# Optimization experiments

Measured on AMD Instinct MI355X. Metric: run time of the kernel, lower is better.

The kernel has to match this reference:

```python
import jax, jax.numpy as jnp
import numpy as np
import math

B, S, IN_DIM, ORIG_DIM, EMBED, HEADS = 8, 1024, 512, 64, 512, 8
HEAD_DIM = EMBED // HEADS


def setup_inputs() -> dict:
    key = jax.random.key(0)
    ks = jax.random.split(key, 4)
    # xavier-uniform-ish init for weights, zero bias (matches _reset_parameters)
    def xavier(k, shape):
        fan_in, fan_out = shape[1], shape[0]
        lim = math.sqrt(6.0 / (fan_in + fan_out))
        return jax.random.uniform(k, shape, jnp.float32, -lim, lim)
    return {
        "x": jax.random.normal(ks[0], (B, S, IN_DIM), jnp.float32),
        "inp": jax.random.normal(ks[1], (B, S, ORIG_DIM), jnp.float32),
        "W_qkv": xavier(ks[2], (3 * EMBED, IN_DIM + ORIG_DIM)),
        "b_qkv": jnp.zeros((3 * EMBED,), jnp.float32),
        "W_o": xavier(ks[3], (EMBED, EMBED)),
        "b_o": jnp.zeros((EMBED,), jnp.float32),
    }


def reference(x, inp, W_qkv, b_qkv, W_o, b_o):
    b, s, _ = x.shape
    xc = jnp.concatenate([x, inp], axis=2)              # [B,S,IN+ORIG]
    qkv = xc @ W_qkv.T + b_qkv                          # [B,S,3E]
    qkv = qkv.reshape(b, s, HEADS, 3 * HEAD_DIM).transpose(0, 2, 1, 3)  # [B,H,S,3d]
    q, k, v = jnp.split(qkv, 3, axis=-1)                # each [B,H,S,d]
    logits = jnp.einsum("bhqd,bhkd->bhqk", q, k) / math.sqrt(HEAD_DIM)
    attention = jax.nn.softmax(logits, axis=-1)         # [B,H,S,S]
    values = jnp.einsum("bhqk,bhkd->bhqd", attention, v)
    values = values.transpose(0, 2, 1, 3).reshape(b, s, EMBED)
    o = values @ W_o.T + b_o                            # [B,S,E]
    return o, attention
```

## Files before the change

### kernel.cpp

```cpp
#include <hip/hip_runtime.h>

typedef __bf16 bf16x8 __attribute__((ext_vector_type(8)));
typedef __bf16 bf16x4 __attribute__((ext_vector_type(4)));
typedef float f32x4 __attribute__((ext_vector_type(4)));

#define MFMA16(a,b,c) __builtin_amdgcn_mfma_f32_16x16x32_bf16((a),(b),(c),0,0,0)

__device__ __forceinline__ void gload_lds16(const void* g, void* l) {
    __builtin_amdgcn_global_load_lds(
        (const __attribute__((address_space(1))) void*)g,
        (__attribute__((address_space(3))) void*)l, 16, 0, 0);
}


__global__ __launch_bounds__(256) void k_convert(
    const float* __restrict__ x, const float* __restrict__ inp,
    const float* __restrict__ Wqkv, const float* __restrict__ Wo,
    __bf16* __restrict__ xc, __bf16* __restrict__ wq, __bf16* __restrict__ wo)
{
    const unsigned C1 = 589824u;
    const unsigned C2 = 110592u;
    unsigned i = blockIdx.x * 256u + threadIdx.x;
    if (i < C1) {
        unsigned e = i * 8u;
        unsigned m = e / 576u, k = e - m * 576u;
        const float* p = (k < 512u) ? x + (size_t)m * 512u + k
                                    : inp + (size_t)m * 64u + (k - 512u);
        f32x4 a = *(const f32x4*)p, b = *(const f32x4*)(p + 4);
        bf16x8 o;
#pragma unroll
        for (int j = 0; j < 4; ++j) { o[j] = (__bf16)a[j]; o[j + 4] = (__bf16)b[j]; }
        *(bf16x8*)&xc[e] = o;
    } else if (i < C1 + C2) {
        unsigned e = (i - C1) * 8u;
        f32x4 a = *(const f32x4*)&Wqkv[e], b = *(const f32x4*)&Wqkv[e + 4];
        bf16x8 o;
#pragma unroll
        for (int j = 0; j < 4; ++j) { o[j] = (__bf16)a[j]; o[j + 4] = (__bf16)b[j]; }
        *(bf16x8*)&wq[e] = o;
    } else {
        unsigned e = (i - C1 - C2) * 8u;
        f32x4 a = *(const f32x4*)&Wo[e], b = *(const f32x4*)&Wo[e + 4];
        bf16x8 o;
#pragma unroll
        for (int j = 0; j < 4; ++j) { o[j] = (__bf16)a[j]; o[j + 4] = (__bf16)b[j]; }
        *(bf16x8*)&wo[e] = o;
    }
}

__global__ __launch_bounds__(256) void k_qkv_gemm(
    const __bf16* __restrict__ A, const __bf16* __restrict__ W,
    const float* __restrict__ bias,
    __bf16* __restrict__ q_ws, __bf16* __restrict__ k_ws, __bf16* __restrict__ vt_ws)
{
    const int K = 576;
    __shared__ __align__(16) __bf16 As[128][32];
    __shared__ __align__(16) __bf16 Bs[128][32];
    int m0 = blockIdx.x * 128, n0 = blockIdx.y * 128;
    int t = threadIdx.x, w = t >> 6, l = t & 63;
    int lo = l & 15, hi = l >> 4;
    int wr = w >> 1, wc = w & 1;

    const __bf16* gA = A + (size_t)(m0 + w * 16 + (l >> 2)) * K + (l & 3) * 8;
    const __bf16* gB = W + (size_t)(n0 + w * 16 + (l >> 2)) * K + (l & 3) * 8;
    char* lA = (char*)&As[0][0] + w * 1024;
    char* lB = (char*)&Bs[0][0] + w * 1024;

    f32x4 acc[4][4] = {};
    for (int k0 = 0; k0 < K; k0 += 32) {
        gload_lds16(gA + k0, lA);
        gload_lds16(gA + 64 * K + k0, lA + 4096);
        gload_lds16(gB + k0, lB);
        gload_lds16(gB + 64 * K + k0, lB + 4096);
        __syncthreads();
        bf16x8 af[4], bq[4];
#pragma unroll
        for (int mi = 0; mi < 4; ++mi) af[mi] = *(const bf16x8*)&As[wr * 64 + mi * 16 + lo][hi * 8];
#pragma unroll
        for (int ni = 0; ni < 4; ++ni) bq[ni] = *(const bf16x8*)&Bs[wc * 64 + ni * 16 + lo][hi * 8];
#pragma unroll
        for (int mi = 0; mi < 4; ++mi)
#pragma unroll
            for (int ni = 0; ni < 4; ++ni)
                acc[mi][ni] = MFMA16(af[mi], bq[ni], acc[mi][ni]);
        __syncthreads();
    }

#pragma unroll
    for (int ni = 0; ni < 4; ++ni) {
        int n = n0 + wc * 64 + ni * 16 + lo;
        int h = n / 192, jj = n % 192, part = jj >> 6, d = jj & 63;
        float bn = bias[n];
#pragma unroll
        for (int mi = 0; mi < 4; ++mi)
#pragma unroll
            for (int j = 0; j < 4; ++j) {
                int m = m0 + wr * 64 + mi * 16 + hi * 4 + j;
                float v = acc[mi][ni][j] + bn;
                int b = m >> 10, s = m & 1023;
                size_t bh = (size_t)(b * 8 + h);
                if (part == 0)      q_ws[(bh * 1024 + s) * 64 + d] = (__bf16)(v * 0.125f);
                else if (part == 1) k_ws[(bh * 1024 + s) * 64 + d] = (__bf16)v;
                else                vt_ws[(bh * 64 + d) * 1024 + s] = (__bf16)v;
            }
    }
}

__global__ __launch_bounds__(256, 4) void k_attn(
    const __bf16* __restrict__ q_ws, const __bf16* __restrict__ k_ws,
    const __bf16* __restrict__ vt_ws,
    float* __restrict__ att_out, __bf16* __restrict__ values)
{
    __shared__ __align__(16) __bf16 Klds[2][64][76];
    __shared__ __align__(16) __bf16 Pl[2][4][16][76];

    int bid = blockIdx.x;
    int nid = (bid & 7) * 128 + (bid >> 3);
    int bh = nid >> 4, qt = nid & 15;
    int t = threadIdx.x, w = t >> 6, l = t & 63;
    int lo = l & 15, hi = l >> 4;
    int q0 = qt * 64 + w * 16;

    const __bf16* Qg = q_ws + ((size_t)bh * 1024 + q0 + lo) * 64 + hi * 8;
    bf16x8 qa0 = *(const bf16x8*)Qg;
    bf16x8 qa1 = *(const bf16x8*)(Qg + 32);

    const __bf16* Kb = k_ws + (size_t)bh * 65536;
    int srow = t >> 2, scol = (t & 3) * 16;
    const __bf16* gK = Kb + (size_t)srow * 64 + scol;
    bf16x8 r0, r1;

#define STAGE_LOAD(c)  { const __bf16* p_ = gK + (size_t)(c) * 4096; \
                         r0 = *(const bf16x8*)p_; r1 = *(const bf16x8*)(p_ + 8); }
#define STAGE_WRITE(b) { *(bf16x8*)&Klds[b][srow][scol] = r0; \
                         *(bf16x8*)&Klds[b][srow][scol + 8] = r1; }
#define SCHUNK(b, s)   _Pragma("unroll") \
                       for (int kk = 0; kk < 4; ++kk) { \
                           bf16x8 kb0 = *(const bf16x8*)&Klds[b][kk * 16 + lo][hi * 8]; \
                           bf16x8 kb1 = *(const bf16x8*)&Klds[b][kk * 16 + lo][hi * 8 + 32]; \
                           f32x4 a_ = {}; \
                           a_ = MFMA16(qa0, kb0, a_); \
                           a_ = MFMA16(qa1, kb1, a_); \
                           s[kk] = a_; \
                       }

    f32x4 lmx = { -3.4e38f, -3.4e38f, -3.4e38f, -3.4e38f };
    f32x4 lsum = {};
    STAGE_LOAD(0); STAGE_WRITE(0);
    __syncthreads();
    for (int c = 0; c < 16; ++c) {
        if (c < 15) STAGE_LOAD(c + 1);
        f32x4 s[4];
        SCHUNK(c & 1, s);
#pragma unroll
        for (int j = 0; j < 4; ++j) {
            float cm = fmaxf(fmaxf(s[0][j], s[1][j]), fmaxf(s[2][j], s[3][j]));
            float nm = fmaxf(lmx[j], cm);
            float a = __expf(s[0][j] - nm) + __expf(s[1][j] - nm)
                    + __expf(s[2][j] - nm) + __expf(s[3][j] - nm);
            lsum[j] = lsum[j] * __expf(lmx[j] - nm) + a;
            lmx[j] = nm;
        }
        if (c < 15) STAGE_WRITE((c + 1) & 1);
        __syncthreads();
    }
    f32x4 gmx = lmx;
#pragma unroll
    for (int off = 1; off < 16; off <<= 1)
#pragma unroll
        for (int j = 0; j < 4; ++j) gmx[j] = fmaxf(gmx[j], __shfl_xor(gmx[j], off));
    f32x4 part;
#pragma unroll
    for (int j = 0; j < 4; ++j) part[j] = lsum[j] * __expf(lmx[j] - gmx[j]);
#pragma unroll
    for (int off = 1; off < 16; off <<= 1)
#pragma unroll
        for (int j = 0; j < 4; ++j) part[j] += __shfl_xor(part[j], off);
    f32x4 ginv;
#pragma unroll
    for (int j = 0; j < 4; ++j) ginv[j] = 1.f / part[j];

    float* gattW = att_out + ((size_t)bh * 1024 + q0) * 1024;
    const __bf16* Vb = vt_ws + (size_t)bh * 65536 + (size_t)(w * 16 + lo) * 1024 + hi * 8;
    f32x4 oacc[4] = {};

    STAGE_LOAD(0); STAGE_WRITE(0);
    __syncthreads();
    for (int c = 0; c < 16; ++c) {
        if (c < 15) STAGE_LOAD(c + 1);
        f32x4 s[4];
        SCHUNK(c & 1, s);
#pragma unroll
        for (int kk = 0; kk < 4; ++kk)
#pragma unroll
            for (int j = 0; j < 4; ++j) {
                float p = __expf(s[kk][j] - gmx[j]) * ginv[j];
                gattW[(size_t)(hi * 4 + j) * 1024 + c * 64 + kk * 16 + lo] = p;
                Pl[c & 1][w][hi * 4 + j][kk * 16 + lo] = (__bf16)p;
            }
        if (c > 0) {
            int pb = (c - 1) & 1;
            const __bf16* vp = Vb + (size_t)(c - 1) * 64;
            bf16x8 vb0 = *(const bf16x8*)vp;
            bf16x8 vb1 = *(const bf16x8*)(vp + 32);
#pragma unroll
            for (int g = 0; g < 4; ++g) {
                bf16x8 pa0 = *(const bf16x8*)&Pl[pb][g][lo][hi * 8];
                bf16x8 pa1 = *(const bf16x8*)&Pl[pb][g][lo][hi * 8 + 32];
                oacc[g] = MFMA16(pa0, vb0, oacc[g]);
                oacc[g] = MFMA16(pa1, vb1, oacc[g]);
            }
        }
        if (c < 15) STAGE_WRITE((c + 1) & 1);
        __syncthreads();
    }
    {
        const __bf16* vp = Vb + (size_t)15 * 64;
        bf16x8 vb0 = *(const bf16x8*)vp;
        bf16x8 vb1 = *(const bf16x8*)(vp + 32);
#pragma unroll
        for (int g = 0; g < 4; ++g) {
            bf16x8 pa0 = *(const bf16x8*)&Pl[1][g][lo][hi * 8];
            bf16x8 pa1 = *(const bf16x8*)&Pl[1][g][lo][hi * 8 + 32];
            oacc[g] = MFMA16(pa0, vb0, oacc[g]);
            oacc[g] = MFMA16(pa1, vb1, oacc[g]);
        }
    }

    int b = bh >> 3, h = bh & 7;
#pragma unroll
    for (int g = 0; g < 4; ++g)
#pragma unroll
        for (int j = 0; j < 4; ++j)
            values[((size_t)b * 1024 + qt * 64 + g * 16 + hi * 4 + j) * 512
                   + h * 64 + w * 16 + lo] = (__bf16)oacc[g][j];
#undef STAGE_LOAD
#undef STAGE_WRITE
#undef SCHUNK
}

__global__ __launch_bounds__(256) void k_out_gemm(
    const __bf16* __restrict__ A, const __bf16* __restrict__ W,
    const float* __restrict__ bias, float* __restrict__ out)
{
    const int K = 512;
    __shared__ __align__(16) __bf16 As[128][32];
    __shared__ __align__(16) __bf16 Bs[128][32];
    int m0 = blockIdx.x * 128, n0 = blockIdx.y * 128;
    int t = threadIdx.x, w = t >> 6, l = t & 63;
    int lo = l & 15, hi = l >> 4;
    int wr = w >> 1, wc = w & 1;

    const __bf16* gA = A + (size_t)(m0 + w * 16 + (l >> 2)) * K + (l & 3) * 8;
    const __bf16* gB = W + (size_t)(n0 + w * 16 + (l >> 2)) * K + (l & 3) * 8;
    char* lA = (char*)&As[0][0] + w * 1024;
    char* lB = (char*)&Bs[0][0] + w * 1024;

    f32x4 acc[4][4] = {};
    for (int k0 = 0; k0 < K; k0 += 32) {
        gload_lds16(gA + k0, lA);
        gload_lds16(gA + 64 * K + k0, lA + 4096);
        gload_lds16(gB + k0, lB);
        gload_lds16(gB + 64 * K + k0, lB + 4096);
        __syncthreads();
        bf16x8 af[4], bq[4];
#pragma unroll
        for (int mi = 0; mi < 4; ++mi) af[mi] = *(const bf16x8*)&As[wr * 64 + mi * 16 + lo][hi * 8];
#pragma unroll
        for (int ni = 0; ni < 4; ++ni) bq[ni] = *(const bf16x8*)&Bs[wc * 64 + ni * 16 + lo][hi * 8];
#pragma unroll
        for (int mi = 0; mi < 4; ++mi)
#pragma unroll
            for (int ni = 0; ni < 4; ++ni)
                acc[mi][ni] = MFMA16(af[mi], bq[ni], acc[mi][ni]);
        __syncthreads();
    }

#pragma unroll
    for (int ni = 0; ni < 4; ++ni) {
        int n = n0 + wc * 64 + ni * 16 + lo;
        float bn = bias[n];
#pragma unroll
        for (int mi = 0; mi < 4; ++mi)
#pragma unroll
            for (int j = 0; j < 4; ++j) {
                int m = m0 + wr * 64 + mi * 16 + hi * 4 + j;
                out[(size_t)m * 512 + n] = acc[mi][ni][j] + bn;
            }
    }
}

extern "C" void kernel_launch(void* const* d_in, const int* in_sizes, int n_in,
                              void* d_out, int out_size, void* d_ws, size_t ws_size,
                              hipStream_t stream)
{
    const float* x    = (const float*)d_in[0];
    const float* inp  = (const float*)d_in[1];
    const float* Wqkv = (const float*)d_in[2];
    const float* bqkv = (const float*)d_in[3];
    const float* Wo   = (const float*)d_in[4];
    const float* bo   = (const float*)d_in[5];

    float* out_o   = (float*)d_out;
    float* out_att = out_o + (size_t)8 * 1024 * 512;

    char* ws = (char*)d_ws;
    __bf16* xc    = (__bf16*)(ws + 0);
    __bf16* wq    = (__bf16*)(ws + 9437184);
    __bf16* wo    = (__bf16*)(ws + 11206656);
    __bf16* q_ws  = (__bf16*)(ws + 11730944);
    __bf16* k_ws  = (__bf16*)(ws + 20119552);
    __bf16* vt_ws = (__bf16*)(ws + 28508160);
    __bf16* vals  = (__bf16*)(ws + 36896768);

    k_convert<<<2864, 256, 0, stream>>>(x, inp, Wqkv, Wo, xc, wq, wo);
    k_qkv_gemm<<<dim3(64, 12), 256, 0, stream>>>(xc, wq, bqkv, q_ws, k_ws, vt_ws);
    k_attn<<<1024, 256, 0, stream>>>(q_ws, k_ws, vt_ws, out_att, vals);
    k_out_gemm<<<dim3(64, 4), 256, 0, stream>>>(vals, wo, bo, out_o);
}
```

Measured before the change: 132.3 us.

## Process two query tiles per attention block, fusing tile B's stats pass with tile A's emit pass

Each attention block now handles two 64-row query tiles of the same head and makes three K sweeps instead of four. Tile B's online max/sum pass is merged into tile A's probability-emit and PV pass, so one K staging serves both. The grid is halved to 512 blocks and the occupancy hint drops from 4 to 2 blocks per CU to allow more registers. The risk is lower parallelism: fewer blocks and fewer waves to hide the latency of the large fp32 attention-matrix stores.

```diff
diff --git a/kernel.cpp b/kernel.cpp
--- a/kernel.cpp
+++ b/kernel.cpp
@@ -106,7 +106,7 @@
     }
 }
 
-__global__ __launch_bounds__(256, 4) void k_attn(
+__global__ __launch_bounds__(256, 2) void k_attn(
     const __bf16* __restrict__ q_ws, const __bf16* __restrict__ k_ws,
     const __bf16* __restrict__ vt_ws,
     float* __restrict__ att_out, __bf16* __restrict__ values)
@@ -115,15 +115,19 @@
     __shared__ __align__(16) __bf16 Pl[2][4][16][76];
 
     int bid = blockIdx.x;
-    int nid = (bid & 7) * 128 + (bid >> 3);
-    int bh = nid >> 4, qt = nid & 15;
+    int nid = (bid & 7) * 64 + (bid >> 3);
+    int bh = nid >> 3, pr = nid & 7;
     int t = threadIdx.x, w = t >> 6, l = t & 63;
     int lo = l & 15, hi = l >> 4;
-    int q0 = qt * 64 + w * 16;
-
-    const __bf16* Qg = q_ws + ((size_t)bh * 1024 + q0 + lo) * 64 + hi * 8;
-    bf16x8 qa0 = *(const bf16x8*)Qg;
-    bf16x8 qa1 = *(const bf16x8*)(Qg + 32);
+    int q0A = pr * 128 + w * 16;
+    int q0B = q0A + 64;
+
+    const __bf16* QgA = q_ws + ((size_t)bh * 1024 + q0A + lo) * 64 + hi * 8;
+    const __bf16* QgB = q_ws + ((size_t)bh * 1024 + q0B + lo) * 64 + hi * 8;
+    bf16x8 qaA0 = *(const bf16x8*)QgA;
+    bf16x8 qaA1 = *(const bf16x8*)(QgA + 32);
+    bf16x8 qaB0 = *(const bf16x8*)QgB;
+    bf16x8 qaB1 = *(const bf16x8*)(QgB + 32);
 
     const __bf16* Kb = k_ws + (size_t)bh * 65536;
     int srow = t >> 2, scol = (t & 3) * 16;
@@ -134,7 +138,7 @@
                          r0 = *(const bf16x8*)p_; r1 = *(const bf16x8*)(p_ + 8); }
 #define STAGE_WRITE(b) { *(bf16x8*)&Klds[b][srow][scol] = r0; \
                          *(bf16x8*)&Klds[b][srow][scol + 8] = r1; }
-#define SCHUNK(b, s)   _Pragma("unroll") \
+#define SCHUNK(b, s, qa0, qa1) _Pragma("unroll") \
                        for (int kk = 0; kk < 4; ++kk) { \
                            bf16x8 kb0 = *(const bf16x8*)&Klds[b][kk * 16 + lo][hi * 8]; \
                            bf16x8 kb1 = *(const bf16x8*)&Klds[b][kk * 16 + lo][hi * 8 + 32]; \
@@ -143,100 +147,126 @@
                            a_ = MFMA16(qa1, kb1, a_); \
                            s[kk] = a_; \
                        }
+#define ONLINE(s, lmx, lsum) _Pragma("unroll") \
+                       for (int j = 0; j < 4; ++j) { \
+                           float cm = fmaxf(fmaxf(s[0][j], s[1][j]), fmaxf(s[2][j], s[3][j])); \
+                           float nm = fmaxf(lmx[j], cm); \
+                           float a = __expf(s[0][j] - nm) + __expf(s[1][j] - nm) \
+                                   + __expf(s[2][j] - nm) + __expf(s[3][j] - nm); \
+                           lsum[j] = lsum[j] * __expf(lmx[j] - nm) + a; \
+                           lmx[j] = nm; \
+                       }
+#define REDUCE(lmx, lsum, gmx, ginv) { \
+                       gmx = lmx; \
+                       _Pragma("unroll") \
+                       for (int off = 1; off < 16; off <<= 1) \
+                           _Pragma("unroll") \
+                           for (int j = 0; j < 4; ++j) gmx[j] = fmaxf(gmx[j], __shfl_xor(gmx[j], off)); \
+                       f32x4 part_; \
+                       _Pragma("unroll") \
+                       for (int j = 0; j < 4; ++j) part_[j] = lsum[j] * __expf(lmx[j] - gmx[j]); \
+                       _Pragma("unroll") \
+                       for (int off = 1; off < 16; off <<= 1) \
+                           _Pragma("unroll") \
+                           for (int j = 0; j < 4; ++j) part_[j] += __shfl_xor(part_[j], off); \
+                       _Pragma("unroll") \
+                       for (int j = 0; j < 4; ++j) ginv[j] = 1.f / part_[j]; }
+#define EMIT(s, gmx, ginv, gatt, pb) _Pragma("unroll") \
+                       for (int kk = 0; kk < 4; ++kk) \
+                           _Pragma("unroll") \
+                           for (int j = 0; j < 4; ++j) { \
+                               float p = __expf(s[kk][j] - gmx[j]) * ginv[j]; \
+                               gatt[(size_t)(hi * 4 + j) * 1024 + c * 64 + kk * 16 + lo] = p; \
+                               Pl[pb][w][hi * 4 + j][kk * 16 + lo] = (__bf16)p; \
+                           }
+#define PV(cc, oacc)   { int pb_ = (cc) & 1; \
+                         const __bf16* vp_ = Vb + (size_t)(cc) * 64; \
+                         bf16x8 vb0 = *(const bf16x8*)vp_; \
+                         bf16x8 vb1 = *(const bf16x8*)(vp_ + 32); \
+                         _Pragma("unroll") \
+                         for (int g = 0; g < 4; ++g) { \
+                             bf16x8 pa0 = *(const bf16x8*)&Pl[pb_][g][lo][hi * 8]; \
+                             bf16x8 pa1 = *(const bf16x8*)&Pl[pb_][g][lo][hi * 8 + 32]; \
+                             oacc[g] = MFMA16(pa0, vb0, oacc[g]); \
+                             oacc[g] = MFMA16(pa1, vb1, oacc[g]); \
+                         } }
+#define VSTORE(qt, oacc) _Pragma("unroll") \
+                       for (int g = 0; g < 4; ++g) \
+                           _Pragma("unroll") \
+                           for (int j = 0; j < 4; ++j) \
+                               values[((size_t)(bh >> 3) * 1024 + (qt) * 64 + g * 16 + hi * 4 + j) * 512 \
+                                      + (bh & 7) * 64 + w * 16 + lo] = (__bf16)oacc[g][j];
+
+    const __bf16* Vb = vt_ws + (size_t)bh * 65536 + (size_t)(w * 16 + lo) * 1024 + hi * 8;
+    float* gattA = att_out + ((size_t)bh * 1024 + q0A) * 1024;
+    float* gattB = att_out + ((size_t)bh * 1024 + q0B) * 1024;
 
     f32x4 lmx = { -3.4e38f, -3.4e38f, -3.4e38f, -3.4e38f };
     f32x4 lsum = {};
+    f32x4 gmxA, ginvA, gmxB, ginvB;
+
     STAGE_LOAD(0); STAGE_WRITE(0);
     __syncthreads();
     for (int c = 0; c < 16; ++c) {
         if (c < 15) STAGE_LOAD(c + 1);
         f32x4 s[4];
-        SCHUNK(c & 1, s);
-#pragma unroll
-        for (int j = 0; j < 4; ++j) {
-            float cm = fmaxf(fmaxf(s[0][j], s[1][j]), fmaxf(s[2][j], s[3][j]));
-            float nm = fmaxf(lmx[j], cm);
-            float a = __expf(s[0][j] - nm) + __expf(s[1][j] - nm)
-                    + __expf(s[2][j] - nm) + __expf(s[3][j] - nm);
-            lsum[j] = lsum[j] * __expf(lmx[j] - nm) + a;
-            lmx[j] = nm;
-        }
+        SCHUNK(c & 1, s, qaA0, qaA1);
+        ONLINE(s, lmx, lsum);
         if (c < 15) STAGE_WRITE((c + 1) & 1);
         __syncthreads();
     }
-    f32x4 gmx = lmx;
-#pragma unroll
-    for (int off = 1; off < 16; off <<= 1)
-#pragma unroll
-        for (int j = 0; j < 4; ++j) gmx[j] = fmaxf(gmx[j], __shfl_xor(gmx[j], off));
-    f32x4 part;
-#pragma unroll
-    for (int j = 0; j < 4; ++j) part[j] = lsum[j] * __expf(lmx[j] - gmx[j]);
-#pragma unroll
-    for (int off = 1; off < 16; off <<= 1)
-#pragma unroll
-        for (int j = 0; j < 4; ++j) part[j] += __shfl_xor(part[j], off);
-    f32x4 ginv;
-#pragma unroll
-    for (int j = 0; j < 4; ++j) ginv[j] = 1.f / part[j];
-
-    float* gattW = att_out + ((size_t)bh * 1024 + q0) * 1024;
-    const __bf16* Vb = vt_ws + (size_t)bh * 65536 + (size_t)(w * 16 + lo) * 1024 + hi * 8;
-    f32x4 oacc[4] = {};
-
+    REDUCE(lmx, lsum, gmxA, ginvA);
+
+    f32x4 oaccA[4] = {};
+#pragma unroll
+    for (int j = 0; j < 4; ++j) { lmx[j] = -3.4e38f; lsum[j] = 0.f; }
     STAGE_LOAD(0); STAGE_WRITE(0);
     __syncthreads();
     for (int c = 0; c < 16; ++c) {
         if (c < 15) STAGE_LOAD(c + 1);
-        f32x4 s[4];
-        SCHUNK(c & 1, s);
-#pragma unroll
-        for (int kk = 0; kk < 4; ++kk)
-#pragma unroll
-            for (int j = 0; j < 4; ++j) {
-                float p = __expf(s[kk][j] - gmx[j]) * ginv[j];
-                gattW[(size_t)(hi * 4 + j) * 1024 + c * 64 + kk * 16 + lo] = p;
-                Pl[c & 1][w][hi * 4 + j][kk * 16 + lo] = (__bf16)p;
-            }
-        if (c > 0) {
-            int pb = (c - 1) & 1;
-            const __bf16* vp = Vb + (size_t)(c - 1) * 64;
-            bf16x8 vb0 = *(const bf16x8*)vp;
-            bf16x8 vb1 = *(const bf16x8*)(vp + 32);
-#pragma unroll
-            for (int g = 0; g < 4; ++g) {
-                bf16x8 pa0 = *(const bf16x8*)&Pl[pb][g][lo][hi * 8];
-                bf16x8 pa1 = *(const bf16x8*)&Pl[pb][g][lo][hi * 8 + 32];
-                oacc[g] = MFMA16(pa0, vb0, oacc[g]);
-                oacc[g] = MFMA16(pa1, vb1, oacc[g]);
-            }
+        {
+            f32x4 s[4];
+            SCHUNK(c & 1, s, qaA0, qaA1);
+            EMIT(s, gmxA, ginvA, gattA, c & 1);
         }
+        {
+            f32x4 s[4];
+            SCHUNK(c & 1, s, qaB0, qaB1);
+            ONLINE(s, lmx, lsum);
+        }
+        if (c > 0) PV(c - 1, oaccA);
         if (c < 15) STAGE_WRITE((c + 1) & 1);
         __syncthreads();
     }
-    {
-        const __bf16* vp = Vb + (size_t)15 * 64;
-        bf16x8 vb0 = *(const bf16x8*)vp;
-        bf16x8 vb1 = *(const bf16x8*)(vp + 32);
-#pragma unroll
-        for (int g = 0; g < 4; ++g) {
-            bf16x8 pa0 = *(const bf16x8*)&Pl[1][g][lo][hi * 8];
-            bf16x8 pa1 = *(const bf16x8*)&Pl[1][g][lo][hi * 8 + 32];
-            oacc[g] = MFMA16(pa0, vb0, oacc[g]);
-            oacc[g] = MFMA16(pa1, vb1, oacc[g]);
+    REDUCE(lmx, lsum, gmxB, ginvB);
+
+    f32x4 oaccB[4] = {};
+    STAGE_LOAD(0); STAGE_WRITE(0);
+    PV(15, oaccA);
+    VSTORE(pr * 2, oaccA);
+    __syncthreads();
+    for (int c = 0; c < 16; ++c) {
+        if (c < 15) STAGE_LOAD(c + 1);
+        {
+            f32x4 s[4];
+            SCHUNK(c & 1, s, qaB0, qaB1);
+            EMIT(s, gmxB, ginvB, gattB, c & 1);
         }
-    }
-
-    int b = bh >> 3, h = bh & 7;
-#pragma unroll
-    for (int g = 0; g < 4; ++g)
-#pragma unroll
-        for (int j = 0; j < 4; ++j)
-            values[((size_t)b * 1024 + qt * 64 + g * 16 + hi * 4 + j) * 512
-                   + h * 64 + w * 16 + lo] = (__bf16)oacc[g][j];
+        if (c > 0) PV(c - 1, oaccB);
+        if (c < 15) STAGE_WRITE((c + 1) & 1);
+        __syncthreads();
+    }
+    PV(15, oaccB);
+    VSTORE(pr * 2 + 1, oaccB);
+
 #undef STAGE_LOAD
 #undef STAGE_WRITE
 #undef SCHUNK
+#undef ONLINE
+#undef REDUCE
+#undef EMIT
+#undef PV
+#undef VSTORE
 }
 
 __global__ __launch_bounds__(256) void k_out_gemm(
@@ -315,6 +345,6 @@
 
     k_convert<<<2864, 256, 0, stream>>>(x, inp, Wqkv, Wo, xc, wq, wo);
     k_qkv_gemm<<<dim3(64, 12), 256, 0, stream>>>(xc, wq, bqkv, q_ws, k_ws, vt_ws);
-    k_attn<<<1024, 256, 0, stream>>>(q_ws, k_ws, vt_ws, out_att, vals);
+    k_attn<<<512, 256, 0, stream>>>(q_ws, k_ws, vt_ws, out_att, vals);
     k_out_gemm<<<dim3(64, 4), 256, 0, stream>>>(vals, wo, bo, out_o);
 }
```

Result: no change. 131.2 us (-0.8%).

## Make attention second pass wave-local with direct K/V loads and exp2 softmax

Applied to the files above, without the earlier changes.

The second pass of the attention kernel drops the shared K staging and block-wide barriers. Each wave now loads K and V fragments straight from global memory and computes P·V only for its own 16 query rows, using a per-wave P buffer in LDS. The log2(e)/sqrt(d) factor is folded into the Q scaling so the softmax can use the native exp2 instruction. The fp32 attention matrix is written with nontemporal stores. The cost is more global and cache traffic for K and V, since the four waves no longer share staged tiles.

```diff
diff --git a/kernel.cpp b/kernel.cpp
--- a/kernel.cpp
+++ b/kernel.cpp
@@ -5,6 +5,8 @@
 typedef float f32x4 __attribute__((ext_vector_type(4)));
 
 #define MFMA16(a,b,c) __builtin_amdgcn_mfma_f32_16x16x32_bf16((a),(b),(c),0,0,0)
+
+__device__ __forceinline__ float fexp2(float x) { return __builtin_amdgcn_exp2f(x); }
 
 __device__ __forceinline__ void gload_lds16(const void* g, void* l) {
     __builtin_amdgcn_global_load_lds(
@@ -99,7 +101,7 @@
                 float v = acc[mi][ni][j] + bn;
                 int b = m >> 10, s = m & 1023;
                 size_t bh = (size_t)(b * 8 + h);
-                if (part == 0)      q_ws[(bh * 1024 + s) * 64 + d] = (__bf16)(v * 0.125f);
+                if (part == 0)      q_ws[(bh * 1024 + s) * 64 + d] = (__bf16)(v * 0.180336881f);
                 else if (part == 1) k_ws[(bh * 1024 + s) * 64 + d] = (__bf16)v;
                 else                vt_ws[(bh * 64 + d) * 1024 + s] = (__bf16)v;
             }
@@ -112,7 +114,7 @@
     float* __restrict__ att_out, __bf16* __restrict__ values)
 {
     __shared__ __align__(16) __bf16 Klds[2][64][76];
-    __shared__ __align__(16) __bf16 Pl[2][4][16][76];
+    __shared__ __align__(16) __bf16 Pl[4][16][76];
 
     int bid = blockIdx.x;
     int nid = (bid & 7) * 128 + (bid >> 3);
@@ -156,9 +158,9 @@
         for (int j = 0; j < 4; ++j) {
             float cm = fmaxf(fmaxf(s[0][j], s[1][j]), fmaxf(s[2][j], s[3][j]));
             float nm = fmaxf(lmx[j], cm);
-            float a = __expf(s[0][j] - nm) + __expf(s[1][j] - nm)
-                    + __expf(s[2][j] - nm) + __expf(s[3][j] - nm);
-            lsum[j] = lsum[j] * __expf(lmx[j] - nm) + a;
+            float a = fexp2(s[0][j] - nm) + fexp2(s[1][j] - nm)
+                    + fexp2(s[2][j] - nm) + fexp2(s[3][j] - nm);
+            lsum[j] = lsum[j] * fexp2(lmx[j] - nm) + a;
             lmx[j] = nm;
         }
         if (c < 15) STAGE_WRITE((c + 1) & 1);
@@ -171,7 +173,7 @@
         for (int j = 0; j < 4; ++j) gmx[j] = fmaxf(gmx[j], __shfl_xor(gmx[j], off));
     f32x4 part;
 #pragma unroll
-    for (int j = 0; j < 4; ++j) part[j] = lsum[j] * __expf(lmx[j] - gmx[j]);
+    for (int j = 0; j < 4; ++j) part[j] = lsum[j] * fexp2(lmx[j] - gmx[j]);
 #pragma unroll
     for (int off = 1; off < 16; off <<= 1)
 #pragma unroll
@@ -181,59 +183,53 @@
     for (int j = 0; j < 4; ++j) ginv[j] = 1.f / part[j];
 
     float* gattW = att_out + ((size_t)bh * 1024 + q0) * 1024;
-    const __bf16* Vb = vt_ws + (size_t)bh * 65536 + (size_t)(w * 16 + lo) * 1024 + hi * 8;
+    const __bf16* Vb = vt_ws + (size_t)bh * 65536;
     f32x4 oacc[4] = {};
 
-    STAGE_LOAD(0); STAGE_WRITE(0);
-    __syncthreads();
     for (int c = 0; c < 16; ++c) {
-        if (c < 15) STAGE_LOAD(c + 1);
         f32x4 s[4];
-        SCHUNK(c & 1, s);
+#pragma unroll
+        for (int kk = 0; kk < 4; ++kk) {
+            const __bf16* kp = Kb + (size_t)(c * 64 + kk * 16 + lo) * 64 + hi * 8;
+            bf16x8 kb0 = *(const bf16x8*)kp;
+            bf16x8 kb1 = *(const bf16x8*)(kp + 32);
+            f32x4 a_ = {};
+            a_ = MFMA16(qa0, kb0, a_);
+            a_ = MFMA16(qa1, kb1, a_);
+            s[kk] = a_;
+        }
+        bf16x8 vb[4][2];
+#pragma unroll
+        for (int dt = 0; dt < 4; ++dt) {
+            const __bf16* vp = Vb + (size_t)(dt * 16 + lo) * 1024 + c * 64 + hi * 8;
+            vb[dt][0] = *(const bf16x8*)vp;
+            vb[dt][1] = *(const bf16x8*)(vp + 32);
+        }
 #pragma unroll
         for (int kk = 0; kk < 4; ++kk)
 #pragma unroll
             for (int j = 0; j < 4; ++j) {
-                float p = __expf(s[kk][j] - gmx[j]) * ginv[j];
-                gattW[(size_t)(hi * 4 + j) * 1024 + c * 64 + kk * 16 + lo] = p;
-                Pl[c & 1][w][hi * 4 + j][kk * 16 + lo] = (__bf16)p;
+                float p = fexp2(s[kk][j] - gmx[j]) * ginv[j];
+                __builtin_nontemporal_store(
+                    p, &gattW[(size_t)(hi * 4 + j) * 1024 + c * 64 + kk * 16 + lo]);
+                Pl[w][hi * 4 + j][kk * 16 + lo] = (__bf16)p;
             }
-        if (c > 0) {
-            int pb = (c - 1) & 1;
-            const __bf16* vp = Vb + (size_t)(c - 1) * 64;
-            bf16x8 vb0 = *(const bf16x8*)vp;
-            bf16x8 vb1 = *(const bf16x8*)(vp + 32);
-#pragma unroll
-            for (int g = 0; g < 4; ++g) {
-                bf16x8 pa0 = *(const bf16x8*)&Pl[pb][g][lo][hi * 8];
-                bf16x8 pa1 = *(const bf16x8*)&Pl[pb][g][lo][hi * 8 + 32];
-                oacc[g] = MFMA16(pa0, vb0, oacc[g]);
-                oacc[g] = MFMA16(pa1, vb1, oacc[g]);
-            }
+        bf16x8 pa0 = *(const bf16x8*)&Pl[w][lo][hi * 8];
+        bf16x8 pa1 = *(const bf16x8*)&Pl[w][lo][32 + hi * 8];
+#pragma unroll
+        for (int dt = 0; dt < 4; ++dt) {
+            oacc[dt] = MFMA16(pa0, vb[dt][0], oacc[dt]);
+            oacc[dt] = MFMA16(pa1, vb[dt][1], oacc[dt]);
         }
-        if (c < 15) STAGE_WRITE((c + 1) & 1);
-        __syncthreads();
-    }
-    {
-        const __bf16* vp = Vb + (size_t)15 * 64;
-        bf16x8 vb0 = *(const bf16x8*)vp;
-        bf16x8 vb1 = *(const bf16x8*)(vp + 32);
-#pragma unroll
-        for (int g = 0; g < 4; ++g) {
-            bf16x8 pa0 = *(const bf16x8*)&Pl[1][g][lo][hi * 8];
-            bf16x8 pa1 = *(const bf16x8*)&Pl[1][g][lo][hi * 8 + 32];
-            oacc[g] = MFMA16(pa0, vb0, oacc[g]);
-            oacc[g] = MFMA16(pa1, vb1, oacc[g]);
-        }
     }
 
     int b = bh >> 3, h = bh & 7;
 #pragma unroll
-    for (int g = 0; g < 4; ++g)
+    for (int dt = 0; dt < 4; ++dt)
 #pragma unroll
         for (int j = 0; j < 4; ++j)
-            values[((size_t)b * 1024 + qt * 64 + g * 16 + hi * 4 + j) * 512
-                   + h * 64 + w * 16 + lo] = (__bf16)oacc[g][j];
+            values[((size_t)b * 1024 + q0 + hi * 4 + j) * 512 + h * 64 + dt * 16 + lo]
+                = (__bf16)oacc[dt][j];
 #undef STAGE_LOAD
 #undef STAGE_WRITE
 #undef SCHUNK
```

New measurement: 186.2 us. 1.41x slower.

## Stream K tiles via direct global-to-LDS loads with XOR swizzle and use exp2

Applied to the files above, without the earlier changes.

The attention kernel now copies each K chunk with direct global-to-LDS loads into an unpadded, XOR-swizzled tile, instead of going through registers into a padded array. The ds reads are swizzled to match. This removes the register staging and LDS store instructions and shrinks LDS use. Separately, the Q pre-scale folds in log2(e) so the softmax can use the hardware exp2 instead of __expf. The kernel is likely bound by writing the fp32 attention matrix, so the gain may be limited.

```diff
diff --git a/kernel.cpp b/kernel.cpp
--- a/kernel.cpp
+++ b/kernel.cpp
@@ -5,6 +5,8 @@
 typedef float f32x4 __attribute__((ext_vector_type(4)));
 
 #define MFMA16(a,b,c) __builtin_amdgcn_mfma_f32_16x16x32_bf16((a),(b),(c),0,0,0)
+
+__device__ __forceinline__ float fexp2(float x) { return __builtin_amdgcn_exp2f(x); }
 
 __device__ __forceinline__ void gload_lds16(const void* g, void* l) {
     __builtin_amdgcn_global_load_lds(
@@ -99,7 +101,7 @@
                 float v = acc[mi][ni][j] + bn;
                 int b = m >> 10, s = m & 1023;
                 size_t bh = (size_t)(b * 8 + h);
-                if (part == 0)      q_ws[(bh * 1024 + s) * 64 + d] = (__bf16)(v * 0.125f);
+                if (part == 0)      q_ws[(bh * 1024 + s) * 64 + d] = (__bf16)(v * 0.180336881f);
                 else if (part == 1) k_ws[(bh * 1024 + s) * 64 + d] = (__bf16)v;
                 else                vt_ws[(bh * 64 + d) * 1024 + s] = (__bf16)v;
             }
@@ -111,7 +113,7 @@
     const __bf16* __restrict__ vt_ws,
     float* __restrict__ att_out, __bf16* __restrict__ values)
 {
-    __shared__ __align__(16) __bf16 Klds[2][64][76];
+    __shared__ __align__(16) __bf16 Klds[2][64][64];
     __shared__ __align__(16) __bf16 Pl[2][4][16][76];
 
     int bid = blockIdx.x;
@@ -126,18 +128,22 @@
     bf16x8 qa1 = *(const bf16x8*)(Qg + 32);
 
     const __bf16* Kb = k_ws + (size_t)bh * 65536;
-    int srow = t >> 2, scol = (t & 3) * 16;
-    const __bf16* gK = Kb + (size_t)srow * 64 + scol;
-    bf16x8 r0, r1;
-
-#define STAGE_LOAD(c)  { const __bf16* p_ = gK + (size_t)(c) * 4096; \
-                         r0 = *(const bf16x8*)p_; r1 = *(const bf16x8*)(p_ + 8); }
-#define STAGE_WRITE(b) { *(bf16x8*)&Klds[b][srow][scol] = r0; \
-                         *(bf16x8*)&Klds[b][srow][scol + 8] = r1; }
+
+    unsigned L0 = (unsigned)(w * 2048 + (l << 4));
+    unsigned L1 = L0 + 1024u;
+    unsigned s0off = (L0 & ~127u) | ((L0 & 127u) ^ (((L0 >> 7) & 7u) << 4));
+    unsigned s1off = (L1 & ~127u) | ((L1 & 127u) ^ (((L1 >> 7) & 7u) << 4));
+
+#define STAGE_GL(c, b) { const char* gc_ = (const char*)Kb + (size_t)(c) * 8192; \
+                         char* lb_ = (char*)&Klds[b][0][0] + w * 2048; \
+                         gload_lds16(gc_ + s0off, lb_); \
+                         gload_lds16(gc_ + s1off, lb_ + 1024); }
 #define SCHUNK(b, s)   _Pragma("unroll") \
                        for (int kk = 0; kk < 4; ++kk) { \
-                           bf16x8 kb0 = *(const bf16x8*)&Klds[b][kk * 16 + lo][hi * 8]; \
-                           bf16x8 kb1 = *(const bf16x8*)&Klds[b][kk * 16 + lo][hi * 8 + 32]; \
+                           const char* kr_ = (const char*)&Klds[b][0][0] + (kk * 16 + lo) * 128; \
+                           unsigned x_ = ((unsigned)(lo & 7)) << 4; \
+                           bf16x8 kb0 = *(const bf16x8*)(kr_ + (((unsigned)(hi * 16)) ^ x_)); \
+                           bf16x8 kb1 = *(const bf16x8*)(kr_ + (((unsigned)(hi * 16 + 64)) ^ x_)); \
                            f32x4 a_ = {}; \
                            a_ = MFMA16(qa0, kb0, a_); \
                            a_ = MFMA16(qa1, kb1, a_); \
@@ -146,22 +152,21 @@
 
     f32x4 lmx = { -3.4e38f, -3.4e38f, -3.4e38f, -3.4e38f };
     f32x4 lsum = {};
-    STAGE_LOAD(0); STAGE_WRITE(0);
+    STAGE_GL(0, 0);
     __syncthreads();
     for (int c = 0; c < 16; ++c) {
-        if (c < 15) STAGE_LOAD(c + 1);
+        if (c < 15) STAGE_GL(c + 1, (c + 1) & 1);
         f32x4 s[4];
         SCHUNK(c & 1, s);
 #pragma unroll
         for (int j = 0; j < 4; ++j) {
             float cm = fmaxf(fmaxf(s[0][j], s[1][j]), fmaxf(s[2][j], s[3][j]));
             float nm = fmaxf(lmx[j], cm);
-            float a = __expf(s[0][j] - nm) + __expf(s[1][j] - nm)
-                    + __expf(s[2][j] - nm) + __expf(s[3][j] - nm);
-            lsum[j] = lsum[j] * __expf(lmx[j] - nm) + a;
+            float a = fexp2(s[0][j] - nm) + fexp2(s[1][j] - nm)
+                    + fexp2(s[2][j] - nm) + fexp2(s[3][j] - nm);
+            lsum[j] = lsum[j] * fexp2(lmx[j] - nm) + a;
             lmx[j] = nm;
         }
-        if (c < 15) STAGE_WRITE((c + 1) & 1);
         __syncthreads();
     }
     f32x4 gmx = lmx;
@@ -171,7 +176,7 @@
         for (int j = 0; j < 4; ++j) gmx[j] = fmaxf(gmx[j], __shfl_xor(gmx[j], off));
     f32x4 part;
 #pragma unroll
-    for (int j = 0; j < 4; ++j) part[j] = lsum[j] * __expf(lmx[j] - gmx[j]);
+    for (int j = 0; j < 4; ++j) part[j] = lsum[j] * fexp2(lmx[j] - gmx[j]);
 #pragma unroll
     for (int off = 1; off < 16; off <<= 1)
 #pragma unroll
@@ -184,17 +189,17 @@
     const __bf16* Vb = vt_ws + (size_t)bh * 65536 + (size_t)(w * 16 + lo) * 1024 + hi * 8;
     f32x4 oacc[4] = {};
 
-    STAGE_LOAD(0); STAGE_WRITE(0);
+    STAGE_GL(0, 0);
     __syncthreads();
     for (int c = 0; c < 16; ++c) {
-        if (c < 15) STAGE_LOAD(c + 1);
+        if (c < 15) STAGE_GL(c + 1, (c + 1) & 1);
         f32x4 s[4];
         SCHUNK(c & 1, s);
 #pragma unroll
         for (int kk = 0; kk < 4; ++kk)
 #pragma unroll
             for (int j = 0; j < 4; ++j) {
-                float p = __expf(s[kk][j] - gmx[j]) * ginv[j];
+                float p = fexp2(s[kk][j] - gmx[j]) * ginv[j];
                 gattW[(size_t)(hi * 4 + j) * 1024 + c * 64 + kk * 16 + lo] = p;
                 Pl[c & 1][w][hi * 4 + j][kk * 16 + lo] = (__bf16)p;
             }
@@ -211,7 +216,6 @@
                 oacc[g] = MFMA16(pa1, vb1, oacc[g]);
             }
         }
-        if (c < 15) STAGE_WRITE((c + 1) & 1);
         __syncthreads();
     }
     {
@@ -234,8 +238,7 @@
         for (int j = 0; j < 4; ++j)
             values[((size_t)b * 1024 + qt * 64 + g * 16 + hi * 4 + j) * 512
                    + h * 64 + w * 16 + lo] = (__bf16)oacc[g][j];
-#undef STAGE_LOAD
-#undef STAGE_WRITE
+#undef STAGE_GL
 #undef SCHUNK
 }
 
```

Result: slower. 136.1 us (+2.9%).
